# Kernel tuning notes

Hardware: AMD Instinct MI355X
Metric: run time of the kernel (lower is better)

Reference implementation:

```python
import jax, jax.numpy as jnp
import numpy as np

B, N, C, D, S, H = 64, 4096, 256, 256, 8, 512
ITERS = 3
EPS = 1e-8
LN_EPS = 1e-3
SCALE = D ** -0.5


def _ln(x, g, b):
    mu = jnp.mean(x, axis=-1, keepdims=True)
    var = jnp.mean((x - mu) ** 2, axis=-1, keepdims=True)
    return (x - mu) * jax.lax.rsqrt(var + LN_EPS) * g + b


def setup_inputs() -> dict:
    key = jax.random.key(0)
    ks = jax.random.split(key, 16)
    limit = np.sqrt(6.0 / (1 + D))
    d = {
        "inputs": jax.random.normal(ks[0], (B, N, C), jnp.float32),
        "noise": jax.random.normal(ks[1], (B, S, D), jnp.float32),
        "slots_mu": jax.random.uniform(ks[2], (1, 1, D), jnp.float32, -limit, limit),
        "slots_log_sigma": jax.random.uniform(ks[3], (1, 1, D), jnp.float32, -limit, limit),
        "Wq": jax.random.normal(ks[4], (D, D), jnp.float32) * (D ** -0.5),
        "Wk": jax.random.normal(ks[5], (D, C), jnp.float32) * (C ** -0.5),
        "Wv": jax.random.normal(ks[6], (D, C), jnp.float32) * (C ** -0.5),
        "W_ih": jax.random.normal(ks[7], (3 * D, D), jnp.float32) * (D ** -0.5),
        "W_hh": jax.random.normal(ks[8], (3 * D, D), jnp.float32) * (D ** -0.5),
        "b_ih": jnp.zeros((3 * D,), jnp.float32),
        "b_hh": jnp.zeros((3 * D,), jnp.float32),
        "mlp_W1": jax.random.normal(ks[9], (H, D), jnp.float32) * (D ** -0.5),
        "mlp_b1": jnp.zeros((H,), jnp.float32),
        "mlp_W2": jax.random.normal(ks[10], (D, H), jnp.float32) * (H ** -0.5),
        "mlp_b2": jnp.zeros((D,), jnp.float32),
        "ln_in_g": jnp.ones((C,), jnp.float32), "ln_in_b": jnp.zeros((C,), jnp.float32),
        "ln_s_g": jnp.ones((D,), jnp.float32), "ln_s_b": jnp.zeros((D,), jnp.float32),
        "ln_ff_g": jnp.ones((D,), jnp.float32), "ln_ff_b": jnp.zeros((D,), jnp.float32),
    }
    return d


def reference(inputs, noise, slots_mu, slots_log_sigma, Wq, Wk, Wv,
              W_ih, W_hh, b_ih, b_hh, mlp_W1, mlp_b1, mlp_W2, mlp_b2,
              ln_in_g, ln_in_b, ln_s_g, ln_s_b, ln_ff_g, ln_ff_b):
    # slot init: mu + exp(log_sigma) * noise  (torch.normal reparameterized)
    slots = slots_mu + jnp.exp(slots_log_sigma) * noise  # [B,S,D]
    x = _ln(inputs, ln_in_g, ln_in_b)
    k = jnp.einsum('bnc,dc->bnd', x, Wk)  # [B,N,D]
    v = jnp.einsum('bnc,dc->bnd', x, Wv)  # [B,N,D]

    for _ in range(ITERS):
        slots_prev = slots
        s = _ln(slots, ln_s_g, ln_s_b)
        q = jnp.einsum('bsd,ed->bse', s, Wq)
        dots = jnp.einsum('bsd,bnd->bsn', q, k) * SCALE  # [B,S,N]
        attn = jax.nn.softmax(dots, axis=1) + EPS  # softmax over SLOT dim
        attn = attn / jnp.sum(attn, axis=-1, keepdims=True)
        updates = jnp.einsum('bnd,bsn->bsd', v, attn)  # [B,S,D]
        # GRUCell(updates, slots_prev)
        gx = updates @ W_ih.T + b_ih  # [B,S,3D]
        gh = slots_prev @ W_hh.T + b_hh
        xr, xz, xn = jnp.split(gx, 3, axis=-1)
        hr, hz, hn = jnp.split(gh, 3, axis=-1)
        r = jax.nn.sigmoid(xr + hr)
        z = jax.nn.sigmoid(xz + hz)
        n = jnp.tanh(xn + r * hn)
        slots = (1.0 - z) * n + z * slots_prev
        # MLP residual
        p = _ln(slots, ln_ff_g, ln_ff_b)
        h1 = jax.nn.relu(p @ mlp_W1.T + mlp_b1)
        slots = slots + h1 @ mlp_W2.T + mlp_b2
    return slots
```

## Files before the change

### kernel.cpp

```cpp
#include <hip/hip_runtime.h>

typedef unsigned short u16;
typedef unsigned int u32;
typedef __attribute__((ext_vector_type(4))) float f32x4;
typedef __attribute__((ext_vector_type(8))) short s16x8;

#define GM 262144
#define GB 64
#define GN 4096
#define GS 8
#define NPART 16

#define GLDS16(G, L) __builtin_amdgcn_global_load_lds( \
    (const __attribute__((address_space(1))) void*)(G), \
    (__attribute__((address_space(3))) void*)(L), 16, 0, 0)

__device__ __forceinline__ float bf2f(u16 u) {
  union { unsigned int i; float f; } c; c.i = ((unsigned int)u) << 16; return c.f;
}
__device__ __forceinline__ u16 f2bf(float f) {
  union { float f; unsigned int i; } c; c.f = f;
  unsigned int x = c.i;
  unsigned int r = x + 0x7FFFu + ((x >> 16) & 1u);
  return (u16)(r >> 16);
}
__device__ __forceinline__ float dot4(f32x4 a, f32x4 b) {
  return a.x*b.x + a.y*b.y + a.z*b.z + a.w*b.w;
}

__global__ void init_slots_kernel(const float* __restrict__ noise, const float* __restrict__ smu,
                                  const float* __restrict__ sls, float* __restrict__ slots)
{
  int i = blockIdx.x * 256 + threadIdx.x;
  int d = i & 255;
  slots[i] = smu[d] + expf(sls[d]) * noise[i];
}

__global__ void wprep_kernel(const float* __restrict__ Wk, const float* __restrict__ Wv,
                             const float* __restrict__ Wih, const float* __restrict__ Whh,
                             const float* __restrict__ W1, const float* __restrict__ W2,
                             u16* __restrict__ wkv, u16* __restrict__ Wcat,
                             u16* __restrict__ W1b, u16* __restrict__ W2b)
{
  int i = blockIdx.x * 256 + threadIdx.x;
  if (i < 131072) {
    wkv[i] = f2bf(i < 65536 ? Wk[i] : Wv[i - 65536]);
  } else if (i < 655360) {
    int j2 = i - 131072;
    int r = j2 >> 9, k = j2 & 511;
    float v;
    if (r < 512)      v = (k < 256) ? Wih[r * 256 + k] : Whh[r * 256 + (k - 256)];
    else if (r < 768) v = (k < 256) ? Wih[r * 256 + k] : 0.f;
    else              v = (k < 256) ? 0.f : Whh[(r - 256) * 256 + (k - 256)];
    Wcat[j2] = f2bf(v);
  } else if (i < 786432) {
    W1b[i - 655360] = f2bf(W1[i - 655360]);
  } else {
    W2b[i - 786432] = f2bf(W2[i - 786432]);
  }
}

__global__ __launch_bounds__(256) void wqk_kernel(
    const float* __restrict__ Wk, const float* __restrict__ Wq,
    float* __restrict__ WqkT, u16* __restrict__ WqkTb)
{
  __shared__ float wkc[256];
  int c = blockIdx.x, t = threadIdx.x;
  wkc[t] = Wk[t * 256 + c];
  __syncthreads();
  float a0 = 0.f, a1 = 0.f, a2 = 0.f, a3 = 0.f;
  #pragma unroll 4
  for (int d = 0; d < 256; d += 4) {
    a0 += wkc[d]     * Wq[(d)     * 256 + t];
    a1 += wkc[d + 1] * Wq[(d + 1) * 256 + t];
    a2 += wkc[d + 2] * Wq[(d + 2) * 256 + t];
    a3 += wkc[d + 3] * Wq[(d + 3) * 256 + t];
  }
  float acc = (a0 + a1 + a2 + a3) * 0.0625f;
  WqkT[c * 256 + t] = acc;
  WqkTb[c * 256 + t] = f2bf(acc);
}

__global__ __launch_bounds__(256) void ln_bf16_kernel(
    const float* __restrict__ x, const float* __restrict__ g, const float* __restrict__ be,
    u16* __restrict__ xbuf)
{
  int row = blockIdx.x * 4 + (threadIdx.x >> 6);
  int lane = threadIdx.x & 63;
  f32x4 v = *(const f32x4*)&x[(size_t)row * 256 + lane * 4];
  float s = v.x + v.y + v.z + v.w;
  float sq = v.x*v.x + v.y*v.y + v.z*v.z + v.w*v.w;
  #pragma unroll
  for (int m = 1; m < 64; m <<= 1) { s += __shfl_xor(s, m, 64); sq += __shfl_xor(sq, m, 64); }
  float mu = s * (1.f / 256.f);
  float var = sq * (1.f / 256.f) - mu * mu;
  float rstd = rsqrtf(var + 1e-3f);
  f32x4 gv = *(const f32x4*)&g[lane * 4];
  f32x4 bv = *(const f32x4*)&be[lane * 4];
  uint2 pk;
  pk.x = (u32)f2bf((v.x - mu) * rstd * gv.x + bv.x)
       | ((u32)f2bf((v.y - mu) * rstd * gv.y + bv.y) << 16);
  pk.y = (u32)f2bf((v.z - mu) * rstd * gv.z + bv.z)
       | ((u32)f2bf((v.w - mu) * rstd * gv.w + bv.w) << 16);
  *(uint2*)&xbuf[(size_t)row * 256 + lane * 4] = pk;
}

__global__ __launch_bounds__(256) void qproj_kernel(const float* __restrict__ slots,
    const float* __restrict__ WqkT,
    const float* __restrict__ g, const float* __restrict__ be, float* __restrict__ gqk)
{
  __shared__ __align__(16) float sl[8][256];
  int b = blockIdx.x, t = threadIdx.x;
  int lane = t & 63, w = t >> 6;
  #pragma unroll
  for (int s2 = 0; s2 < 2; ++s2) {
    int s = w * 2 + s2;
    f32x4 v = *(const f32x4*)&slots[(size_t)(b * 8 + s) * 256 + lane * 4];
    float s1 = v.x + v.y + v.z + v.w;
    float q1 = v.x*v.x + v.y*v.y + v.z*v.z + v.w*v.w;
    #pragma unroll
    for (int m = 1; m < 64; m <<= 1) { s1 += __shfl_xor(s1, m, 64); q1 += __shfl_xor(q1, m, 64); }
    float mu = s1 * (1.f / 256.f);
    float var = q1 * (1.f / 256.f) - mu * mu;
    float rstd = rsqrtf(var + 1e-3f);
    f32x4 gv = *(const f32x4*)&g[lane * 4];
    f32x4 bv = *(const f32x4*)&be[lane * 4];
    f32x4 o;
    o.x = (v.x - mu) * rstd * gv.x + bv.x;
    o.y = (v.y - mu) * rstd * gv.y + bv.y;
    o.z = (v.z - mu) * rstd * gv.z + bv.z;
    o.w = (v.w - mu) * rstd * gv.w + bv.w;
    *(f32x4*)&sl[s][lane * 4] = o;
  }
  __syncthreads();
  float a[8];
  #pragma unroll
  for (int s = 0; s < 8; ++s) a[s] = 0.f;
  const f32x4* wr = (const f32x4*)&WqkT[(size_t)t * 256];
  for (int k = 0; k < 64; ++k) {
    f32x4 w4 = wr[k];
    #pragma unroll
    for (int s = 0; s < 8; ++s) a[s] += dot4(w4, *(const f32x4*)&sl[s][k * 4]);
  }
  #pragma unroll
  for (int s = 0; s < 8; ++s) gqk[(size_t)(b * 8 + s) * 256 + t] = a[s];
}

__global__ __launch_bounds__(256) void attn_kernel(
    const u16* __restrict__ xb, const float* __restrict__ gqk,
    float* __restrict__ gUp, float* __restrict__ gdp)
{
  __shared__ __align__(16) u16 X[2 * 64 * 256];
  __shared__ __align__(16) u16 P[16 * 72];
  __shared__ float denL[4][8];
  const int b = blockIdx.y, chunk = blockIdx.x;
  const int t = threadIdx.x;
  const int lane = t & 63, w = t >> 6;
  const int fr = lane & 15, fq = lane >> 4;
  const bool valid = fr < 8;

  for (int i = t; i < 288; i += 256) ((u32*)P)[288 + i] = 0;

  {
    const u16* src = xb + ((size_t)b * 4096 + (size_t)(chunk * 4) * 64) * 256;
    #pragma unroll
    for (int p = 0; p < 8; ++p) {
      int q = p * 256 + t;
      int n = q >> 5, cl = q & 31;
      int fn = ((n >> 1) & 4) | ((n >> 3) & 2);
      GLDS16(src + (size_t)n * 256 + ((cl ^ fn) * 8), &X[q * 8]);
    }
  }

  s16x8 qf[8];
  if (valid) {
    const float* qr = gqk + (size_t)b * 2048 + fr * 256;
    #pragma unroll
    for (int ks = 0; ks < 8; ++ks) {
      f32x4 a = *(const f32x4*)&qr[ks * 32 + fq * 8];
      f32x4 c = *(const f32x4*)&qr[ks * 32 + fq * 8 + 4];
      s16x8 q8;
      q8[0] = (short)f2bf(a.x); q8[1] = (short)f2bf(a.y);
      q8[2] = (short)f2bf(a.z); q8[3] = (short)f2bf(a.w);
      q8[4] = (short)f2bf(c.x); q8[5] = (short)f2bf(c.y);
      q8[6] = (short)f2bf(c.z); q8[7] = (short)f2bf(c.w);
      qf[ks] = q8;
    }
  } else {
    #pragma unroll
    for (int ks = 0; ks < 8; ++ks) { s16x8 z = {0,0,0,0,0,0,0,0}; qf[ks] = z; }
  }

  const int fnA = ((fr >> 1) & 4) | ((w & 1) << 1);
  const int fnB = ((fq & 1) << 2) | ((fq >> 1) << 1);

  float denom_loc = 0.f;
  f32x4 uacc[4];
  #pragma unroll
  for (int ct = 0; ct < 4; ++ct) { f32x4 z = {0.f,0.f,0.f,0.f}; uacc[ct] = z; }

  #pragma unroll
  for (int ti = 0; ti < 4; ++ti) {
    __builtin_amdgcn_s_barrier();
    __builtin_amdgcn_sched_barrier(0);
    if (ti < 3) {
      const u16* src = xb + ((size_t)b * 4096 + (size_t)(chunk * 4 + ti + 1) * 64) * 256;
      u16* dstb = &X[((ti + 1) & 1) * 16384];
      #pragma unroll
      for (int p = 0; p < 8; ++p) {
        int q = p * 256 + t;
        int n = q >> 5, cl = q & 31;
        int fn = ((n >> 1) & 4) | ((n >> 3) & 2);
        GLDS16(src + (size_t)n * 256 + ((cl ^ fn) * 8), dstb + q * 8);
      }
      asm volatile("s_waitcnt vmcnt(8)" ::: "memory");
    } else {
      asm volatile("s_waitcnt vmcnt(0)" ::: "memory");
    }
    __builtin_amdgcn_sched_barrier(0);
    __builtin_amdgcn_s_barrier();
    __builtin_amdgcn_sched_barrier(0);

    const u16* Xc = &X[(ti & 1) * 16384];

    f32x4 dacc = {0.f, 0.f, 0.f, 0.f};
    {
      const u16* xrow = &Xc[(w * 16 + fr) * 256];
      #pragma unroll
      for (int ks = 0; ks < 8; ++ks) {
        s16x8 a = *(const s16x8*)&xrow[(((ks * 4 + fq) ^ fnA) * 8)];
        dacc = __builtin_amdgcn_mfma_f32_16x16x32_bf16(a, qf[ks], dacc, 0, 0, 0);
      }
    }
    float pw[4];
    #pragma unroll
    for (int r = 0; r < 4; ++r) {
      float d = dacc[r];
      float m = d;
      #pragma unroll
      for (int msk = 1; msk < 8; msk <<= 1) m = fmaxf(m, __shfl_xor(m, msk, 64));
      float e = expf(d - m);
      float sm = e;
      #pragma unroll
      for (int msk = 1; msk < 8; msk <<= 1) sm += __shfl_xor(sm, msk, 64);
      pw[r] = valid ? (e / sm + 1e-8f) : 0.f;
    }
    denom_loc += pw[0] + pw[1] + pw[2] + pw[3];
    if (valid) {
      u32* p32 = (u32*)P;
      int pi = fr * 36 + w * 8 + fq * 2;
      p32[pi]     = (u32)f2bf(pw[0]) | ((u32)f2bf(pw[1]) << 16);
      p32[pi + 1] = (u32)f2bf(pw[2]) | ((u32)f2bf(pw[3]) << 16);
    }
    asm volatile("s_waitcnt lgkmcnt(0)" ::: "memory");
    __builtin_amdgcn_sched_barrier(0);
    __builtin_amdgcn_s_barrier();
    __builtin_amdgcn_sched_barrier(0);

    #pragma unroll
    for (int ch = 0; ch < 2; ++ch) {
      s16x8 pa = *(const s16x8*)&P[fr * 72 + ch * 32 + fq * 8];
      #pragma unroll
      for (int ct = 0; ct < 4; ++ct) {
        int c = w * 64 + ct * 16 + fr;
        const u16* xcol = &Xc[(ch * 32 + fq * 8) * 256 + (((c >> 3) ^ fnB) * 8) + (c & 7)];
        union { s16x8 v; u32 u[4]; } vb;
        #pragma unroll
        for (int jj = 0; jj < 4; ++jj) {
          u16 e0 = xcol[(jj * 2) * 256];
          u16 e1 = xcol[(jj * 2 + 1) * 256];
          vb.u[jj] = (u32)e0 | ((u32)e1 << 16);
        }
        uacc[ct] = __builtin_amdgcn_mfma_f32_16x16x32_bf16(pa, vb.v, uacc[ct], 0, 0, 0);
      }
    }
  }

  float dl = denom_loc;
  dl += __shfl_xor(dl, 16, 64);
  dl += __shfl_xor(dl, 32, 64);
  if (lane < 8) denL[w][lane] = dl;
  if (fq < 2) {
    size_t obase = (size_t)(b * NPART + chunk) * 2048;
    #pragma unroll
    for (int ct = 0; ct < 4; ++ct)
      #pragma unroll
      for (int r = 0; r < 4; ++r)
        gUp[obase + (size_t)(fq * 4 + r) * 256 + w * 64 + ct * 16 + fr] = uacc[ct][r];
  }
  __syncthreads();
  if (t < 8) gdp[(b * NPART + chunk) * 8 + t] = denL[0][t] + denL[1][t] + denL[2][t] + denL[3][t];
}

__global__ __launch_bounds__(256) void update_kernel(
    const float* __restrict__ gUp, const float* __restrict__ gdp,
    float* __restrict__ slots,
    const u16* __restrict__ WvB,
    const u16* __restrict__ Wcat, const float* __restrict__ b_ih, const float* __restrict__ b_hh,
    const u16* __restrict__ W1b, const float* __restrict__ b1,
    const u16* __restrict__ W2b, const float* __restrict__ b2,
    const float* __restrict__ lng, const float* __restrict__ lnb,
    const u16* __restrict__ WqkTb, const float* __restrict__ lnsg, const float* __restrict__ lnsb,
    float* __restrict__ gqk, float* __restrict__ out, int last)
{
  __shared__ __align__(16) u16 bufA[16 * 520];
  __shared__ __align__(16) u16 bufP[16 * 264];
  __shared__ __align__(16) u16 bufU[16 * 264];
  __shared__ float g[1024 * 10];
  __shared__ float nl[8 * 256];
  __shared__ float sp[8 * 256];
  __shared__ float scr[16];
  const int b = blockIdx.x;
  const int t = threadIdx.x;
  const int lane = t & 63, w = t >> 6;
  const int fr = lane & 15, fq = lane >> 4;

  #pragma unroll
  for (int s = 0; s < 8; ++s) {
    float den = 0.f, ua = 0.f;
    #pragma unroll 4
    for (int c = 0; c < NPART; ++c) {
      den += gdp[(b * NPART + c) * 8 + s];
      ua  += gUp[(size_t)(b * NPART + c) * 2048 + s * 256 + t];
    }
    bufU[s * 264 + t] = f2bf(ua / den);
    float spv = slots[(b * 8 + s) * 256 + t];
    bufA[s * 520 + 256 + t] = f2bf(spv);
    sp[s * 256 + t] = spv;
  }
  for (int i = t; i < 8 * 520; i += 256) bufA[8 * 520 + i] = 0;
  for (int i = t; i < 8 * 264; i += 256) { bufP[8 * 264 + i] = 0; bufU[8 * 264 + i] = 0; }
  __syncthreads();

  {
    s16x8 pa[8];
    #pragma unroll
    for (int ks = 0; ks < 8; ++ks)
      pa[ks] = *(const s16x8*)&bufU[fr * 264 + ks * 32 + fq * 8];
    for (int nf = 0; nf < 4; ++nf) {
      int n0 = w * 64 + nf * 16;
      f32x4 acc = {0.f, 0.f, 0.f, 0.f};
      #pragma unroll
      for (int ks = 0; ks < 8; ++ks) {
        s16x8 bb = *(const s16x8*)&WvB[(size_t)(n0 + fr) * 256 + ks * 32 + fq * 8];
        acc = __builtin_amdgcn_mfma_f32_16x16x32_bf16(pa[ks], bb, acc, 0, 0, 0);
      }
      if (fq < 2) {
        int d = n0 + fr;
        #pragma unroll
        for (int r = 0; r < 4; ++r)
          bufA[(fq * 4 + r) * 520 + d] = f2bf(acc[r]);
      }
    }
  }
  __syncthreads();

  {
    s16x8 afr[16];
    #pragma unroll
    for (int ks = 0; ks < 16; ++ks)
      afr[ks] = *(const s16x8*)&bufA[fr * 520 + ks * 32 + fq * 8];
    for (int nf = 0; nf < 16; ++nf) {
      int n0 = w * 256 + nf * 16;
      f32x4 acc = {0.f, 0.f, 0.f, 0.f};
      #pragma unroll
      for (int ks = 0; ks < 16; ++ks) {
        s16x8 bb = *(const s16x8*)&Wcat[(size_t)(n0 + fr) * 512 + ks * 32 + fq * 8];
        acc = __builtin_amdgcn_mfma_f32_16x16x32_bf16(afr[ks], bb, acc, 0, 0, 0);
      }
      if (fq < 2) {
        int j = n0 + fr;
        #pragma unroll
        for (int r = 0; r < 4; ++r) g[j * 10 + fq * 4 + r] = acc[r];
      }
    }
  }
  __syncthreads();

  {
    float bi0 = b_ih[t],       bh0 = b_hh[t];
    float bi1 = b_ih[256 + t], bh1 = b_hh[256 + t];
    float bi2 = b_ih[512 + t], bh2 = b_hh[512 + t];
    #pragma unroll
    for (int s = 0; s < 8; ++s) {
      float rr = 1.f / (1.f + expf(-(g[t * 10 + s] + bi0 + bh0)));
      float z  = 1.f / (1.f + expf(-(g[(256 + t) * 10 + s] + bi1 + bh1)));
      float xn = g[(512 + t) * 10 + s] + bi2;
      float hn = g[(768 + t) * 10 + s] + bh2;
      float nn = tanhf(xn + rr * hn);
      nl[s * 256 + t] = (1.f - z) * nn + z * sp[s * 256 + t];
    }
  }
  __syncthreads();

  {
    int ln_ = t & 63;
    #pragma unroll
    for (int j = 0; j < 2; ++j) {
      int sl = w * 2 + j;
      f32x4 v = *(const f32x4*)&nl[sl * 256 + ln_ * 4];
      float s1 = v.x + v.y + v.z + v.w;
      float s2 = v.x*v.x + v.y*v.y + v.z*v.z + v.w*v.w;
      #pragma unroll
      for (int m = 1; m < 64; m <<= 1) { s1 += __shfl_xor(s1, m, 64); s2 += __shfl_xor(s2, m, 64); }
      if (ln_ == 0) {
        float mu = s1 * (1.f / 256.f);
        float var = s2 * (1.f / 256.f) - mu * mu;
        scr[sl * 2] = mu;
        scr[sl * 2 + 1] = rsqrtf(var + 1e-3f);
      }
    }
  }
  __syncthreads();
  {
    float lg = lng[t], lb = lnb[t];
    #pragma unroll
    for (int s = 0; s < 8; ++s)
      bufP[s * 264 + t] = f2bf((nl[s * 256 + t] - scr[s * 2]) * scr[s * 2 + 1] * lg + lb);
  }
  __syncthreads();

  {
    s16x8 pa[8];
    #pragma unroll
    for (int ks = 0; ks < 8; ++ks)
      pa[ks] = *(const s16x8*)&bufP[fr * 264 + ks * 32 + fq * 8];
    for (int nf = 0; nf < 8; ++nf) {
      int n0 = w * 128 + nf * 16;
      f32x4 acc = {0.f, 0.f, 0.f, 0.f};
      #pragma unroll
      for (int ks = 0; ks < 8; ++ks) {
        s16x8 bb = *(const s16x8*)&W1b[(size_t)(n0 + fr) * 256 + ks * 32 + fq * 8];
        acc = __builtin_amdgcn_mfma_f32_16x16x32_bf16(pa[ks], bb, acc, 0, 0, 0);
      }
      if (fq < 2) {
        float bb1 = b1[n0 + fr];
        #pragma unroll
        for (int r = 0; r < 4; ++r)
          bufA[(fq * 4 + r) * 520 + n0 + fr] = f2bf(fmaxf(acc[r] + bb1, 0.f));
      }
    }
  }
  __syncthreads();

  {
    s16x8 ha[16];
    #pragma unroll
    for (int ks = 0; ks < 16; ++ks)
      ha[ks] = *(const s16x8*)&bufA[fr * 520 + ks * 32 + fq * 8];
    for (int nf = 0; nf < 4; ++nf) {
      int n0 = w * 64 + nf * 16;
      f32x4 acc = {0.f, 0.f, 0.f, 0.f};
      #pragma unroll
      for (int ks = 0; ks < 16; ++ks) {
        s16x8 bb = *(const s16x8*)&W2b[(size_t)(n0 + fr) * 512 + ks * 32 + fq * 8];
        acc = __builtin_amdgcn_mfma_f32_16x16x32_bf16(ha[ks], bb, acc, 0, 0, 0);
      }
      if (fq < 2) {
        int d = n0 + fr;
        float bb2 = b2[d];
        #pragma unroll
        for (int r = 0; r < 4; ++r) {
          int sl = fq * 4 + r;
          float val = acc[r] + nl[sl * 256 + d] + bb2;
          slots[(b * 8 + sl) * 256 + d] = val;
          sp[sl * 256 + d] = val;
          if (last) out[(b * 8 + sl) * 256 + d] = val;
        }
      }
    }
  }
  if (last) return;
  __syncthreads();

  {
    int ln_ = t & 63;
    #pragma unroll
    for (int j = 0; j < 2; ++j) {
      int sl = w * 2 + j;
      f32x4 v = *(const f32x4*)&sp[sl * 256 + ln_ * 4];
      float s1 = v.x + v.y + v.z + v.w;
      float s2 = v.x*v.x + v.y*v.y + v.z*v.z + v.w*v.w;
      #pragma unroll
      for (int m = 1; m < 64; m <<= 1) { s1 += __shfl_xor(s1, m, 64); s2 += __shfl_xor(s2, m, 64); }
      if (ln_ == 0) {
        float mu = s1 * (1.f / 256.f);
        float var = s2 * (1.f / 256.f) - mu * mu;
        scr[sl * 2] = mu;
        scr[sl * 2 + 1] = rsqrtf(var + 1e-3f);
      }
    }
  }
  __syncthreads();
  {
    float lg = lnsg[t], lb = lnsb[t];
    #pragma unroll
    for (int s = 0; s < 8; ++s)
      bufP[s * 264 + t] = f2bf((sp[s * 256 + t] - scr[s * 2]) * scr[s * 2 + 1] * lg + lb);
  }
  __syncthreads();
  {
    s16x8 pa[8];
    #pragma unroll
    for (int ks = 0; ks < 8; ++ks)
      pa[ks] = *(const s16x8*)&bufP[fr * 264 + ks * 32 + fq * 8];
    for (int nf = 0; nf < 4; ++nf) {
      int n0 = w * 64 + nf * 16;
      f32x4 acc = {0.f, 0.f, 0.f, 0.f};
      #pragma unroll
      for (int ks = 0; ks < 8; ++ks) {
        s16x8 bb = *(const s16x8*)&WqkTb[(size_t)(n0 + fr) * 256 + ks * 32 + fq * 8];
        acc = __builtin_amdgcn_mfma_f32_16x16x32_bf16(pa[ks], bb, acc, 0, 0, 0);
      }
      if (fq < 2) {
        int e = n0 + fr;
        #pragma unroll
        for (int r = 0; r < 4; ++r)
          gqk[(size_t)(b * 8 + fq * 4 + r) * 256 + e] = acc[r];
      }
    }
  }
}

extern "C" void kernel_launch(void* const* d_in, const int* in_sizes, int n_in,
                              void* d_out, int out_size, void* d_ws, size_t ws_size,
                              hipStream_t stream) {
  const float* inputs   = (const float*)d_in[0];
  const float* noise    = (const float*)d_in[1];
  const float* slots_mu = (const float*)d_in[2];
  const float* slots_ls = (const float*)d_in[3];
  const float* Wq   = (const float*)d_in[4];
  const float* Wk   = (const float*)d_in[5];
  const float* Wv   = (const float*)d_in[6];
  const float* W_ih = (const float*)d_in[7];
  const float* W_hh = (const float*)d_in[8];
  const float* b_ih = (const float*)d_in[9];
  const float* b_hh = (const float*)d_in[10];
  const float* W1   = (const float*)d_in[11];
  const float* b1   = (const float*)d_in[12];
  const float* W2   = (const float*)d_in[13];
  const float* b2   = (const float*)d_in[14];
  const float* ln_in_g = (const float*)d_in[15];
  const float* ln_in_b = (const float*)d_in[16];
  const float* ln_s_g  = (const float*)d_in[17];
  const float* ln_s_b  = (const float*)d_in[18];
  const float* ln_ff_g = (const float*)d_in[19];
  const float* ln_ff_b = (const float*)d_in[20];
  float* out = (float*)d_out;

  char* w = (char*)d_ws;
  u16* xbuf = (u16*)w;      w += (size_t)GM * 256 * 2;
  float* gUp = (float*)w;
  float* gdp = (float*)(w + (size_t)GB * NPART * 2048 * 4);
  w += (size_t)GB * NPART * 2048 * 4 + (size_t)GB * NPART * 8 * 4 + 4096;
  u16* wkv = (u16*)w;       w += (size_t)512 * 256 * 2;
  u16* Wcat = (u16*)w;      w += (size_t)1024 * 512 * 2;
  u16* W1b = (u16*)w;       w += (size_t)512 * 256 * 2;
  u16* W2b = (u16*)w;       w += (size_t)256 * 512 * 2;
  float* WqkT = (float*)w;  w += (size_t)256 * 256 * 4;
  u16* WqkTb = (u16*)w;     w += (size_t)256 * 256 * 2;
  float* slots = (float*)w; w += (size_t)131072 * 4;
  float* gqk = (float*)w;   w += (size_t)131072 * 4;

  u16* WvB = wkv + 65536;

  init_slots_kernel<<<512, 256, 0, stream>>>(noise, slots_mu, slots_ls, slots);
  wprep_kernel<<<3584, 256, 0, stream>>>(Wk, Wv, W_ih, W_hh, W1, W2, wkv, Wcat, W1b, W2b);
  wqk_kernel<<<256, 256, 0, stream>>>(Wk, Wq, WqkT, WqkTb);
  ln_bf16_kernel<<<GM / 4, 256, 0, stream>>>(inputs, ln_in_g, ln_in_b, xbuf);

  qproj_kernel<<<64, 256, 0, stream>>>(slots, WqkT, ln_s_g, ln_s_b, gqk);
  for (int it = 0; it < 3; ++it) {
    attn_kernel<<<dim3(NPART, GB), 256, 0, stream>>>(xbuf, gqk, gUp, gdp);
    update_kernel<<<64, 256, 0, stream>>>(gUp, gdp, slots, WvB, Wcat, b_ih, b_hh,
                                          W1b, b1, W2b, b2, ln_ff_g, ln_ff_b,
                                          WqkTb, ln_s_g, ln_s_b, gqk, out, it == 2);
  }
}
```

Baseline: 512.2 us.

## Replace async global-to-LDS double buffer with register prefetch and single LDS buffer

Attention-kernel tile loads now go through registers instead of global_load_lds directly into LDS. The next tile is prefetched into VGPRs during compute and written to a single LDS buffer after each tile. This halves LDS use (32KB to 16KB) to allow more blocks per CU. It costs extra VGPRs for the prefetch, one more barrier pair per tile, and it drops the full unroll of the tile loop.

```diff
diff --git a/kernel.cpp b/kernel.cpp
--- a/kernel.cpp
+++ b/kernel.cpp
@@ -10,10 +10,6 @@
 #define GN 4096
 #define GS 8
 #define NPART 16
-
-#define GLDS16(G, L) __builtin_amdgcn_global_load_lds( \
-    (const __attribute__((address_space(1))) void*)(G), \
-    (__attribute__((address_space(3))) void*)(L), 16, 0, 0)
 
 __device__ __forceinline__ float bf2f(u16 u) {
   union { unsigned int i; float f; } c; c.i = ((unsigned int)u) << 16; return c.f;
@@ -150,7 +146,7 @@
     const u16* __restrict__ xb, const float* __restrict__ gqk,
     float* __restrict__ gUp, float* __restrict__ gdp)
 {
-  __shared__ __align__(16) u16 X[2 * 64 * 256];
+  __shared__ __align__(16) u16 X[64 * 256];
   __shared__ __align__(16) u16 P[16 * 72];
   __shared__ float denL[4][8];
   const int b = blockIdx.y, chunk = blockIdx.x;
@@ -161,16 +157,20 @@
 
   for (int i = t; i < 288; i += 256) ((u32*)P)[288 + i] = 0;
 
-  {
-    const u16* src = xb + ((size_t)b * 4096 + (size_t)(chunk * 4) * 64) * 256;
-    #pragma unroll
-    for (int p = 0; p < 8; ++p) {
-      int q = p * 256 + t;
-      int n = q >> 5, cl = q & 31;
-      int fn = ((n >> 1) & 4) | ((n >> 3) & 2);
-      GLDS16(src + (size_t)n * 256 + ((cl ^ fn) * 8), &X[q * 8]);
-    }
-  }
+  int off[8];
+  #pragma unroll
+  for (int p = 0; p < 8; ++p) {
+    int q = p * 256 + t;
+    int n = q >> 5, cl = q & 31;
+    int fn = ((n >> 1) & 4) | ((n >> 3) & 2);
+    off[p] = n * 256 + ((cl ^ fn) * 8);
+  }
+
+  const u16* xbase = xb + (size_t)b * 4096 * 256 + (size_t)chunk * 4 * 64 * 256;
+
+  uint4 pf[8];
+  #pragma unroll
+  for (int p = 0; p < 8; ++p) pf[p] = *(const uint4*)(xbase + off[p]);
 
   s16x8 qf[8];
   if (valid) {
@@ -191,6 +191,15 @@
     for (int ks = 0; ks < 8; ++ks) { s16x8 z = {0,0,0,0,0,0,0,0}; qf[ks] = z; }
   }
 
+  asm volatile("s_waitcnt vmcnt(0)" ::: "memory");
+  __builtin_amdgcn_sched_barrier(0);
+  #pragma unroll
+  for (int p = 0; p < 8; ++p) *(uint4*)&X[(p * 256 + t) * 8] = pf[p];
+  asm volatile("s_waitcnt lgkmcnt(0)" ::: "memory");
+  __builtin_amdgcn_sched_barrier(0);
+  __builtin_amdgcn_s_barrier();
+  __builtin_amdgcn_sched_barrier(0);
+
   const int fnA = ((fr >> 1) & 4) | ((w & 1) << 1);
   const int fnB = ((fq & 1) << 2) | ((fq >> 1) << 1);
 
@@ -199,33 +208,17 @@
   #pragma unroll
   for (int ct = 0; ct < 4; ++ct) { f32x4 z = {0.f,0.f,0.f,0.f}; uacc[ct] = z; }
 
-  #pragma unroll
   for (int ti = 0; ti < 4; ++ti) {
-    __builtin_amdgcn_s_barrier();
+    if (ti < 3) {
+      const u16* src = xbase + (size_t)(ti + 1) * 16384;
+      #pragma unroll
+      for (int p = 0; p < 8; ++p) pf[p] = *(const uint4*)(src + off[p]);
+    }
     __builtin_amdgcn_sched_barrier(0);
-    if (ti < 3) {
-      const u16* src = xb + ((size_t)b * 4096 + (size_t)(chunk * 4 + ti + 1) * 64) * 256;
-      u16* dstb = &X[((ti + 1) & 1) * 16384];
-      #pragma unroll
-      for (int p = 0; p < 8; ++p) {
-        int q = p * 256 + t;
-        int n = q >> 5, cl = q & 31;
-        int fn = ((n >> 1) & 4) | ((n >> 3) & 2);
-        GLDS16(src + (size_t)n * 256 + ((cl ^ fn) * 8), dstb + q * 8);
-      }
-      asm volatile("s_waitcnt vmcnt(8)" ::: "memory");
-    } else {
-      asm volatile("s_waitcnt vmcnt(0)" ::: "memory");
-    }
-    __builtin_amdgcn_sched_barrier(0);
-    __builtin_amdgcn_s_barrier();
-    __builtin_amdgcn_sched_barrier(0);
-
-    const u16* Xc = &X[(ti & 1) * 16384];
 
     f32x4 dacc = {0.f, 0.f, 0.f, 0.f};
     {
-      const u16* xrow = &Xc[(w * 16 + fr) * 256];
+      const u16* xrow = &X[(w * 16 + fr) * 256];
       #pragma unroll
       for (int ks = 0; ks < 8; ++ks) {
         s16x8 a = *(const s16x8*)&xrow[(((ks * 4 + fq) ^ fnA) * 8)];
@@ -263,7 +256,7 @@
       #pragma unroll
       for (int ct = 0; ct < 4; ++ct) {
         int c = w * 64 + ct * 16 + fr;
-        const u16* xcol = &Xc[(ch * 32 + fq * 8) * 256 + (((c >> 3) ^ fnB) * 8) + (c & 7)];
+        const u16* xcol = &X[(ch * 32 + fq * 8) * 256 + (((c >> 3) ^ fnB) * 8) + (c & 7)];
         union { s16x8 v; u32 u[4]; } vb;
         #pragma unroll
         for (int jj = 0; jj < 4; ++jj) {
@@ -273,6 +266,19 @@
         }
         uacc[ct] = __builtin_amdgcn_mfma_f32_16x16x32_bf16(pa, vb.v, uacc[ct], 0, 0, 0);
       }
+    }
+
+    if (ti < 3) {
+      __builtin_amdgcn_s_barrier();
+      __builtin_amdgcn_sched_barrier(0);
+      asm volatile("s_waitcnt vmcnt(0)" ::: "memory");
+      __builtin_amdgcn_sched_barrier(0);
+      #pragma unroll
+      for (int p = 0; p < 8; ++p) *(uint4*)&X[(p * 256 + t) * 8] = pf[p];
+      asm volatile("s_waitcnt lgkmcnt(0)" ::: "memory");
+      __builtin_amdgcn_sched_barrier(0);
+      __builtin_amdgcn_s_barrier();
+      __builtin_amdgcn_sched_barrier(0);
     }
   }
 
```

Measured after the change: 635.1 us. 1.24x slower.
